# Kernel optimization log

Hardware: AMD Instinct MI355X
Metric: run time of the kernel (lower is better)

## Reference

```python
import jax, jax.numpy as jnp
import numpy as np

E = 2048
H = 16
D = E // H  # head_dim = 128


def setup_inputs() -> dict:
    key = jax.random.key(0)
    ks = jax.random.split(key, 8)
    s = 0.02
    x = jax.random.normal(ks[0], (2, 2048, E), dtype=jnp.float32)
    Wq = jax.random.normal(ks[1], (E, E), dtype=jnp.float32) * s
    Wk = jax.random.normal(ks[2], (E, E), dtype=jnp.float32) * s
    Wv = jax.random.normal(ks[3], (E, E), dtype=jnp.float32) * s
    W1 = jax.random.normal(ks[4], (2 * E, E), dtype=jnp.float32) * s
    b1 = jax.random.normal(ks[5], (2 * E,), dtype=jnp.float32) * s
    W2 = jax.random.normal(ks[6], (E, 2 * E), dtype=jnp.float32) * s
    b2 = jax.random.normal(ks[7], (E,), dtype=jnp.float32) * s
    return {"x": x, "Wq": Wq, "Wk": Wk, "Wv": Wv, "W1": W1, "b1": b1, "W2": W2, "b2": b2}


def reference(x, Wq, Wk, Wv, W1, b1, W2, b2):
    B, S, _ = x.shape
    # QKV projections (torch Linear: x @ W.T), reshape to (B,S,H,D)
    q = (x @ Wq.T).reshape(B, S, H, D)
    k = (x @ Wk.T).reshape(B, S, H, D)
    v = (x @ Wv.T).reshape(B, S, H, D)
    # scores: (B,H,S,S)
    score = jnp.einsum('bqhd,bkhd->bhqk', q, k)
    # causal mask added BEFORE scaling (as in original; -inf unaffected by scale)
    causal = jnp.tril(jnp.ones((S, S), dtype=bool))
    score = jnp.where(causal, score, -jnp.inf)
    score = score / jnp.sqrt(jnp.float32(D))
    attn = jax.nn.softmax(score, axis=-1)
    o = jnp.einsum('bhqk,bkhd->bqhd', attn, v).reshape(B, S, E)
    # FFN with hidden = 2*E, no residual connections in this block
    h = jax.nn.gelu(o @ W1.T + b1)
    return h @ W2.T + b2
```

## Files before the change

kernel.cpp:

```cpp
#include <hip/hip_runtime.h>
#include <cmath>


typedef _Float16 half8 __attribute__((ext_vector_type(8)));
typedef _Float16 half4v __attribute__((ext_vector_type(4)));
typedef float float4v __attribute__((ext_vector_type(4)));

__device__ inline void load_lds16(const _Float16* g, _Float16* l) {
  __builtin_amdgcn_global_load_lds(
      (const __attribute__((address_space(1))) void*)g,
      (__attribute__((address_space(3))) void*)l, 16, 0, 0);
}

__global__ void cvt_kernel(const float* __restrict__ s0, const float* __restrict__ s1,
                           const float* __restrict__ s2, const float* __restrict__ s3,
                           _Float16* d0, _Float16* d1, _Float16* d2, _Float16* d3,
                           int n0, int n1, int n2, int n3, float sc1) {
  const float* s;
  _Float16* d;
  int n;
  float sc = 1.0f;
  switch (blockIdx.y) {
    case 0: s = s0; d = d0; n = n0; break;
    case 1: s = s1; d = d1; n = n1; sc = sc1; break;
    case 2: s = s2; d = d2; n = n2; break;
    default: s = s3; d = d3; n = n3; break;
  }
  const int step = gridDim.x * 256 * 4;
  for (int i = (blockIdx.x * 256 + threadIdx.x) * 4; i < n; i += step) {
    float4v v = *(const float4v*)&s[i];
    half4v h;
#pragma unroll
    for (int e = 0; e < 4; e++) h[e] = (_Float16)(v[e] * sc);
    *(half4v*)&d[i] = h;
  }
}

__device__ __forceinline__ void gemm8_core(
    const _Float16* __restrict__ A, const _Float16* __restrict__ B, int K,
    int bm, int bn, _Float16* lds, float4v acc[8][4]) {
  const int tid = threadIdx.x;
  const int w = tid >> 6, lane = tid & 63;
  const int l16 = lane & 15, quad = lane >> 4;
  const int srow = w * 16 + (lane >> 2);
  const int clocal = ((lane & 3) * 8) ^ ((lane & 32) ? 16 : 0);
  int rdh = (l16 << 5) + (quad << 3);
  rdh ^= (l16 & 8) << 1;

  const _Float16* pA0 = A + (size_t)(bm + srow) * K + clocal;
  const _Float16* pA1 = A + (size_t)(bm + 128 + srow) * K + clocal;
  const _Float16* pB0 = B + (size_t)(bn + srow) * K + clocal;
  const _Float16* pB1 = B + (size_t)(bn + 128 + srow) * K + clocal;

  _Float16* const dA0 = lds + w * 1024;
  _Float16* const dA1 = lds + 8192 + w * 1024;
  _Float16* const dB0 = lds + 16384 + w * 1024;
  _Float16* const dB1 = lds + 24576 + w * 1024;

  const int aH = w >> 2, bH = (w >> 1) & 1, bRB = (w & 1) * 4;
  const _Float16* const rA0 = lds + aH * 8192;
  const _Float16* const rB0 = lds + 16384 + bH * 8192;
  const _Float16* const rA1 = rA0 + 32768;
  const _Float16* const rB1 = rB0 + 32768;

  const int NT = K >> 6;

#define STG(p, d, kt)                     \
  do {                                    \
    const _Float16* _s = (p) + (kt) * 64; \
    load_lds16(_s, (d));                  \
    load_lds16(_s + 32, (d) + 512);       \
  } while (0)
#define BARRIER() asm volatile("s_barrier" ::: "memory")
#define WAIT_LGKM()                                  \
  asm volatile("s_waitcnt lgkmcnt(0)" ::: "memory"); \
  __builtin_amdgcn_sched_barrier(0);
#define RD_A(base, RB0)                                                       \
  _Pragma("unroll") for (int rb = 0; rb < 4; rb++)                            \
  _Pragma("unroll") for (int ks = 0; ks < 2; ks++)                            \
      af[rb][ks] = *(const half8*)&(base)[((((RB0) + rb) * 2 + ks) << 9) + rdh];
#define RD_B(base, J0)                                                        \
  _Pragma("unroll") for (int j = 0; j < 2; j++)                               \
  _Pragma("unroll") for (int ks = 0; ks < 2; ks++)                            \
      bf[(J0) + j][ks] =                                                      \
          *(const half8*)&(base)[(((bRB + (J0) + j) * 2 + ks) << 9) + rdh];
#define MFMA_Q(RB0, J0)                                                       \
  __builtin_amdgcn_s_setprio(1);                                              \
  _Pragma("unroll") for (int rb = 0; rb < 4; rb++)                            \
  _Pragma("unroll") for (int j = 0; j < 2; j++)                               \
  _Pragma("unroll") for (int ks = 0; ks < 2; ks++)                            \
      acc[(RB0) + rb][(J0) + j] = __builtin_amdgcn_mfma_f32_16x16x32_f16(     \
          af[rb][ks], bf[(J0) + j][ks], acc[(RB0) + rb][(J0) + j], 0, 0, 0);  \
  __builtin_amdgcn_s_setprio(0);                                              \
  BARRIER();

  STG(pB0, dB0, 0); STG(pB1, dB1, 0); STG(pA0, dA0, 0); STG(pA1, dA1, 0);
  STG(pB0, dB0 + 32768, 1); STG(pB1, dB1 + 32768, 1);
  asm volatile("s_waitcnt vmcnt(4)" ::: "memory");
  BARRIER();

  half8 af[4][2], bf[4][2];

  for (int t = 0; t < NT; t += 2) {
    const bool last = (t + 2 >= NT);
    RD_A(rA0, 0) RD_B(rB0, 0)
    STG(pA0, dA0 + 32768, t + 1);
    BARRIER(); WAIT_LGKM()
    MFMA_Q(0, 0)
    RD_B(rB0, 2)
    STG(pA1, dA1 + 32768, t + 1);
    BARRIER(); WAIT_LGKM()
    MFMA_Q(0, 2)
    RD_A(rA0, 4)
    if (!last) STG(pB0, dB0, t + 2);
    BARRIER(); WAIT_LGKM()
    MFMA_Q(4, 0)
    if (!last) {
      STG(pA0, dA0, t + 2);
      asm volatile("s_waitcnt vmcnt(4)" ::: "memory");
    } else {
      asm volatile("s_waitcnt vmcnt(0)" ::: "memory");
    }
    BARRIER();
    MFMA_Q(4, 2)
    RD_A(rA1, 0) RD_B(rB1, 0)
    if (!last) STG(pA1, dA1, t + 2);
    BARRIER(); WAIT_LGKM()
    MFMA_Q(0, 0)
    RD_B(rB1, 2)
    if (!last) STG(pB1, dB1, t + 2);
    BARRIER(); WAIT_LGKM()
    MFMA_Q(0, 2)
    RD_A(rA1, 4)
    if (!last) STG(pB0, dB0 + 32768, t + 3);
    BARRIER(); WAIT_LGKM()
    MFMA_Q(4, 0)
    if (!last) {
      STG(pB1, dB1 + 32768, t + 3);
      asm volatile("s_waitcnt vmcnt(4)" ::: "memory");
    }
    BARRIER();
    MFMA_Q(4, 2)
  }
#undef STG
#undef BARRIER
#undef WAIT_LGKM
#undef RD_A
#undef RD_B
#undef MFMA_Q
}

__global__ __launch_bounds__(512, 2) void gemm_qkv(
    const _Float16* __restrict__ xh, const _Float16* __restrict__ Wq,
    const _Float16* __restrict__ Wk, const _Float16* __restrict__ Wv,
    _Float16* __restrict__ Qh, _Float16* __restrict__ Kh,
    _Float16* __restrict__ Vt) {
  __shared__ __align__(16) _Float16 lds[65536];
  const int z = blockIdx.z;
  const _Float16* B = (z == 0) ? Wq : (z == 1 ? Wk : Wv);
  const int bm = blockIdx.y * 256, bn = blockIdx.x * 256;
  float4v acc[8][4] = {};
  gemm8_core(xh, B, 2048, bm, bn, lds, acc);

  const int tid = threadIdx.x;
  const int w = tid >> 6, lane = tid & 63;
  const int l16 = lane & 15, quad = lane >> 4;
  const int wm = (w >> 2) * 128, wn = (w & 3) * 64;
  _Float16* outRM = z ? Kh : Qh;
#pragma unroll
  for (int j = 0; j < 4; j++) {
    const int col = bn + wn + j * 16 + l16;
#pragma unroll
    for (int rb = 0; rb < 8; rb++) {
      const int rbase = bm + wm + rb * 16 + quad * 4;
#pragma unroll
      for (int reg = 0; reg < 4; reg++) {
        const int m = rbase + reg;
        const _Float16 hv = (_Float16)acc[rb][j][reg];
        if (z == 2)
          Vt[((size_t)(m >> 11) << 22) + ((size_t)col << 11) + (m & 2047)] = hv;
        else
          outRM[(size_t)m * 2048 + col] = hv;
      }
    }
  }
}

template <bool GELU>
__global__ __launch_bounds__(512, 2) void gemm_ffn(
    const _Float16* __restrict__ A, const _Float16* __restrict__ B,
    const float* __restrict__ bias, void* __restrict__ out, int N, int K) {
  __shared__ __align__(16) _Float16 lds[65536];
  const int bm = blockIdx.y * 256, bn = blockIdx.x * 256;
  float4v acc[8][4] = {};
  gemm8_core(A, B, K, bm, bn, lds, acc);

  const int tid = threadIdx.x;
  const int w = tid >> 6, lane = tid & 63;
  const int l16 = lane & 15, quad = lane >> 4;
  const int wm = (w >> 2) * 128, wn = (w & 3) * 64;
#pragma unroll
  for (int j = 0; j < 4; j++) {
    const int col = bn + wn + j * 16 + l16;
    const float bv = bias[col];
#pragma unroll
    for (int rb = 0; rb < 8; rb++) {
      const int rbase = bm + wm + rb * 16 + quad * 4;
#pragma unroll
      for (int reg = 0; reg < 4; reg++) {
        const int m = rbase + reg;
        float v = acc[rb][j][reg] + bv;
        if (GELU) {
          const float x = v;
          const float inner = 0.7978845608028654f * (x + 0.044715f * x * x * x);
          v = 0.5f * x * (1.0f + tanhf(inner));
          ((_Float16*)out)[(size_t)m * N + col] = (_Float16)v;
        } else {
          ((float*)out)[(size_t)m * N + col] = v;
        }
      }
    }
  }
}

__global__ __launch_bounds__(256, 2) void attn_mfma(
    const _Float16* __restrict__ Qh, const _Float16* __restrict__ Kh,
    const _Float16* __restrict__ Vt, _Float16* __restrict__ Oh) {
  __shared__ __align__(16) _Float16 Ksh[64][136];
  __shared__ __align__(16) _Float16 Vsh[128][72];
  __shared__ __align__(16) _Float16 Psh[4][32][72];

  const int b = blockIdx.z;
  int qt = blockIdx.x;
  if (b) qt = gridDim.x - 1 - qt;
  const int h = blockIdx.y;
  const int tid = threadIdx.x;
  const int wave = tid >> 6, lane = tid & 63;
  const int l16 = lane & 15, quad = lane >> 4;
  const int q0 = qt * 128;
  const int wq0 = q0 + wave * 32;

  half8 qf[2][4];
#pragma unroll
  for (int rb = 0; rb < 2; rb++)
#pragma unroll
    for (int kc = 0; kc < 4; kc++)
      qf[rb][kc] = *(const half8*)(Qh +
          (size_t)(b * 2048 + wq0 + rb * 16 + l16) * 2048 + h * 128 +
          kc * 32 + quad * 8);

  half8 ones;
#pragma unroll
  for (int e = 0; e < 8; e++) ones[e] = (_Float16)1.0f;

  const int kkey = tid >> 2, kd = (tid & 3) * 32;
  const int vd = tid >> 1, vkey = (tid & 1) * 32;

  half8 kpre[4], vpre[4];
  {
    const _Float16* p = Kh + (size_t)(b * 2048 + kkey) * 2048 + h * 128 + kd;
#pragma unroll
    for (int i = 0; i < 4; i++) kpre[i] = *(const half8*)(p + i * 8);
    const _Float16* pv = Vt + ((size_t)b << 22) + (size_t)(h * 128 + vd) * 2048 + vkey;
#pragma unroll
    for (int i = 0; i < 4; i++) vpre[i] = *(const half8*)(pv + i * 8);
  }

  float4v o[2][9] = {};
  float4v mrow[2];
#pragma unroll
  for (int rb = 0; rb < 2; rb++)
#pragma unroll
    for (int e = 0; e < 4; e++) mrow[rb][e] = -INFINITY;

  const int nkb = qt * 2 + 2;
  for (int kb = 0; kb < nkb; kb++) {
    const int k0 = kb * 64;
    __syncthreads();
#pragma unroll
    for (int i = 0; i < 4; i++) *(half8*)&Ksh[kkey][kd + i * 8] = kpre[i];
#pragma unroll
    for (int i = 0; i < 4; i++) *(half8*)&Vsh[vd][vkey + i * 8] = vpre[i];
    __syncthreads();

    if (kb + 1 < nkb) {
      const int k1 = k0 + 64;
      const _Float16* p = Kh + (size_t)(b * 2048 + k1 + kkey) * 2048 + h * 128 + kd;
#pragma unroll
      for (int i = 0; i < 4; i++) kpre[i] = *(const half8*)(p + i * 8);
      const _Float16* pv = Vt + ((size_t)b << 22) + (size_t)(h * 128 + vd) * 2048 + k1 + vkey;
#pragma unroll
      for (int i = 0; i < 4; i++) vpre[i] = *(const half8*)(pv + i * 8);
    }

    if (k0 <= wq0 + 31) {
      float4v s[2][4] = {};
#pragma unroll
      for (int kc = 0; kc < 4; kc++) {
#pragma unroll
        for (int cb = 0; cb < 4; cb++) {
          half8 kf = *(const half8*)&Ksh[cb * 16 + l16][kc * 32 + quad * 8];
#pragma unroll
          for (int rb = 0; rb < 2; rb++)
            s[rb][cb] = __builtin_amdgcn_mfma_f32_16x16x32_f16(qf[rb][kc], kf, s[rb][cb], 0, 0, 0);
        }
      }
      if (k0 + 63 > wq0) {
#pragma unroll
        for (int cb = 0; cb < 4; cb++)
#pragma unroll
          for (int rb = 0; rb < 2; rb++)
#pragma unroll
            for (int reg = 0; reg < 4; reg++) {
              const int key = k0 + cb * 16 + l16;
              const int row = wq0 + rb * 16 + quad * 4 + reg;
              if (key > row) s[rb][cb][reg] = -INFINITY;
            }
      }
#pragma unroll
      for (int rb = 0; rb < 2; rb++) {
        float4v mt;
#pragma unroll
        for (int e = 0; e < 4; e++)
          mt[e] = fmaxf(fmaxf(s[rb][0][e], s[rb][1][e]),
                        fmaxf(s[rb][2][e], s[rb][3][e]));
#pragma unroll
        for (int msk = 1; msk <= 8; msk <<= 1)
#pragma unroll
          for (int e = 0; e < 4; e++) mt[e] = fmaxf(mt[e], __shfl_xor(mt[e], msk, 64));
        int need = 0;
#pragma unroll
        for (int e = 0; e < 4; e++) need |= (mt[e] > mrow[rb][e] + 8.0f) ? 1 : 0;
        if (__any(need)) {
          float4v al;
#pragma unroll
          for (int e = 0; e < 4; e++) {
            const float mn = fmaxf(mrow[rb][e], mt[e]);
            al[e] = exp2f(mrow[rb][e] - mn);
            mrow[rb][e] = mn;
          }
#pragma unroll
          for (int cd = 0; cd < 9; cd++)
#pragma unroll
            for (int e = 0; e < 4; e++) o[rb][cd][e] *= al[e];
        }
#pragma unroll
        for (int cb = 0; cb < 4; cb++) {
#pragma unroll
          for (int e = 0; e < 4; e++) s[rb][cb][e] = exp2f(s[rb][cb][e] - mrow[rb][e]);
#pragma unroll
          for (int e = 0; e < 4; e++)
            Psh[wave][rb * 16 + quad * 4 + e][cb * 16 + l16] = (_Float16)s[rb][cb][e];
        }
      }
      half8 pf[2][2];
#pragma unroll
      for (int rb = 0; rb < 2; rb++)
#pragma unroll
        for (int kc = 0; kc < 2; kc++)
          pf[rb][kc] = *(const half8*)&Psh[wave][rb * 16 + l16][kc * 32 + quad * 8];
#pragma unroll
      for (int cd = 0; cd < 8; cd++) {
#pragma unroll
        for (int kc = 0; kc < 2; kc++) {
          half8 vf = *(const half8*)&Vsh[cd * 16 + l16][kc * 32 + quad * 8];
#pragma unroll
          for (int rb = 0; rb < 2; rb++)
            o[rb][cd] = __builtin_amdgcn_mfma_f32_16x16x32_f16(pf[rb][kc], vf, o[rb][cd], 0, 0, 0);
        }
      }
#pragma unroll
      for (int kc = 0; kc < 2; kc++)
#pragma unroll
        for (int rb = 0; rb < 2; rb++)
          o[rb][8] = __builtin_amdgcn_mfma_f32_16x16x32_f16(pf[rb][kc], ones, o[rb][8], 0, 0, 0);
    }
  }

#pragma unroll
  for (int rb = 0; rb < 2; rb++) {
    float4v inv;
#pragma unroll
    for (int e = 0; e < 4; e++) inv[e] = 1.0f / o[rb][8][e];
#pragma unroll
    for (int cd = 0; cd < 8; cd++)
#pragma unroll
      for (int reg = 0; reg < 4; reg++)
        Oh[(size_t)(b * 2048 + wq0 + rb * 16 + quad * 4 + reg) * 2048 +
           h * 128 + cd * 16 + l16] = (_Float16)(o[rb][cd][reg] * inv[reg]);
  }
}

extern "C" void kernel_launch(void* const* d_in, const int* in_sizes, int n_in,
                              void* d_out, int out_size, void* d_ws,
                              size_t ws_size, hipStream_t stream) {
  const float* x = (const float*)d_in[0];
  const float* Wq = (const float*)d_in[1];
  const float* Wk = (const float*)d_in[2];
  const float* Wv = (const float*)d_in[3];
  const float* W1 = (const float*)d_in[4];
  const float* b1 = (const float*)d_in[5];
  const float* W2 = (const float*)d_in[6];
  const float* b2 = (const float*)d_in[7];
  float* out = (float*)d_out;

  const int ME = 8388608;
  const int EE = 4194304;

  _Float16* ws = (_Float16*)d_ws;
  _Float16* xh  = ws;
  _Float16* Wqh = xh + ME;
  _Float16* Wkh = Wqh + EE;
  _Float16* Wvh = Wkh + EE;
  _Float16* Qh  = Wvh + EE;
  _Float16* Kh  = Qh + ME;
  _Float16* Vt  = Kh + ME;
  _Float16* Oh  = xh;
  _Float16* W1h = Wqh;
  _Float16* W2h = Vt;
  _Float16* Hid = Qh;

  const float qscale = 1.4426950408889634f * 0.08838834764831845f;

  cvt_kernel<<<dim3(1024, 4), 256, 0, stream>>>(x, Wq, Wk, Wv, xh, Wqh, Wkh, Wvh,
                                                ME, EE, EE, EE, qscale);
  gemm_qkv<<<dim3(8, 16, 3), 512, 0, stream>>>(xh, Wqh, Wkh, Wvh, Qh, Kh, Vt);
  attn_mfma<<<dim3(16, 16, 2), 256, 0, stream>>>(Qh, Kh, Vt, Oh);
  cvt_kernel<<<dim3(1024, 2), 256, 0, stream>>>(W1, W2, nullptr, nullptr,
                                                W1h, W2h, nullptr, nullptr,
                                                ME, ME, 0, 0, 1.0f);
  gemm_ffn<true><<<dim3(16, 16), 512, 0, stream>>>(Oh, W1h, b1, Hid, 4096, 2048);
  gemm_ffn<false><<<dim3(8, 16), 512, 0, stream>>>(Hid, W2h, b2, out, 2048, 4096);
}
```

Baseline: 601.6 us.

## Restructure GEMM pipeline with double-buffered fragments, XCD tile swizzle, LDS-staged V transpose

Rewrites the GEMM main loop to keep low and high register fragment sets, so LDS reads for the next MFMA quarter overlap the current one. It uses partial lgkmcnt waits and fewer barriers, and issues global-to-LDS copies in pairs. Block indices are remapped so consecutive tiles land on the same XCD for L2 reuse. The V projection epilogue now transposes through padded LDS and writes vectorised rows instead of scattered scalar stores, at the cost of extra registers and a slightly larger LDS allocation.

Result: slower. 671.0 us (+11.5%).

```diff
diff --git a/kernel.cpp b/kernel.cpp
--- a/kernel.cpp
+++ b/kernel.cpp
@@ -36,6 +36,36 @@
   }
 }
 
+#define STG2(p, d, kt)                    \
+  do {                                    \
+    const _Float16* _s = (p) + (kt) * 64; \
+    load_lds16(_s, (d));                  \
+    load_lds16(_s + 32, (d) + 512);       \
+  } while (0)
+#define BAR() asm volatile("s_barrier" ::: "memory")
+#define SB0() __builtin_amdgcn_sched_barrier(0)
+#define VM0() asm volatile("s_waitcnt vmcnt(0)" ::: "memory")
+#define WAITL(N)                                          \
+  asm volatile("s_waitcnt lgkmcnt(" #N ")" ::: "memory"); \
+  __builtin_amdgcn_sched_barrier(0);
+#define RD_AF(dst, base, RB0)                                                \
+  _Pragma("unroll") for (int rb = 0; rb < 4; rb++)                           \
+  _Pragma("unroll") for (int ks = 0; ks < 2; ks++)                           \
+      dst[rb][ks] = *(const half8*)&(base)[((((RB0) + rb) * 2 + ks) << 9) + rdh];
+#define RD_BF(dst, base, J0)                                                 \
+  _Pragma("unroll") for (int j = 0; j < 2; j++)                              \
+  _Pragma("unroll") for (int ks = 0; ks < 2; ks++)                           \
+      dst[j][ks] =                                                           \
+          *(const half8*)&(base)[(((bRB + (J0) + j) * 2 + ks) << 9) + rdh];
+#define MFMA16(AF, BF, RB0, J0)                                              \
+  __builtin_amdgcn_s_setprio(1);                                             \
+  _Pragma("unroll") for (int rb = 0; rb < 4; rb++)                           \
+  _Pragma("unroll") for (int j = 0; j < 2; j++)                              \
+  _Pragma("unroll") for (int ks = 0; ks < 2; ks++)                           \
+      acc[(RB0) + rb][(J0) + j] = __builtin_amdgcn_mfma_f32_16x16x32_f16(    \
+          AF[rb][ks], BF[j][ks], acc[(RB0) + rb][(J0) + j], 0, 0, 0);        \
+  __builtin_amdgcn_s_setprio(0);
+
 __device__ __forceinline__ void gemm8_core(
     const _Float16* __restrict__ A, const _Float16* __restrict__ B, int K,
     int bm, int bn, _Float16* lds, float4v acc[8][4]) {
@@ -58,96 +88,79 @@
   _Float16* const dB1 = lds + 24576 + w * 1024;
 
   const int aH = w >> 2, bH = (w >> 1) & 1, bRB = (w & 1) * 4;
-  const _Float16* const rA0 = lds + aH * 8192;
-  const _Float16* const rB0 = lds + 16384 + bH * 8192;
-  const _Float16* const rA1 = rA0 + 32768;
-  const _Float16* const rB1 = rB0 + 32768;
+  const _Float16* const rA = lds + aH * 8192;
+  const _Float16* const rB = lds + 16384 + bH * 8192;
+  const _Float16* const rAn = rA + 32768;
+  const _Float16* const rBn = rB + 32768;
 
   const int NT = K >> 6;
 
-#define STG(p, d, kt)                     \
-  do {                                    \
-    const _Float16* _s = (p) + (kt) * 64; \
-    load_lds16(_s, (d));                  \
-    load_lds16(_s + 32, (d) + 512);       \
-  } while (0)
-#define BARRIER() asm volatile("s_barrier" ::: "memory")
-#define WAIT_LGKM()                                  \
-  asm volatile("s_waitcnt lgkmcnt(0)" ::: "memory"); \
-  __builtin_amdgcn_sched_barrier(0);
-#define RD_A(base, RB0)                                                       \
-  _Pragma("unroll") for (int rb = 0; rb < 4; rb++)                            \
-  _Pragma("unroll") for (int ks = 0; ks < 2; ks++)                            \
-      af[rb][ks] = *(const half8*)&(base)[((((RB0) + rb) * 2 + ks) << 9) + rdh];
-#define RD_B(base, J0)                                                        \
-  _Pragma("unroll") for (int j = 0; j < 2; j++)                               \
-  _Pragma("unroll") for (int ks = 0; ks < 2; ks++)                            \
-      bf[(J0) + j][ks] =                                                      \
-          *(const half8*)&(base)[(((bRB + (J0) + j) * 2 + ks) << 9) + rdh];
-#define MFMA_Q(RB0, J0)                                                       \
-  __builtin_amdgcn_s_setprio(1);                                              \
-  _Pragma("unroll") for (int rb = 0; rb < 4; rb++)                            \
-  _Pragma("unroll") for (int j = 0; j < 2; j++)                               \
-  _Pragma("unroll") for (int ks = 0; ks < 2; ks++)                            \
-      acc[(RB0) + rb][(J0) + j] = __builtin_amdgcn_mfma_f32_16x16x32_f16(     \
-          af[rb][ks], bf[(J0) + j][ks], acc[(RB0) + rb][(J0) + j], 0, 0, 0);  \
-  __builtin_amdgcn_s_setprio(0);                                              \
-  BARRIER();
-
-  STG(pB0, dB0, 0); STG(pB1, dB1, 0); STG(pA0, dA0, 0); STG(pA1, dA1, 0);
-  STG(pB0, dB0 + 32768, 1); STG(pB1, dB1 + 32768, 1);
+  half8 afLo[4][2], afHi[4][2], bfLo[2][2], bfHi[2][2];
+
+  STG2(pB0, dB0, 0); STG2(pB1, dB1, 0); STG2(pA0, dA0, 0); STG2(pA1, dA1, 0);
+  STG2(pB0, dB0 + 32768, 1); STG2(pB1, dB1 + 32768, 1);
   asm volatile("s_waitcnt vmcnt(4)" ::: "memory");
-  BARRIER();
-
-  half8 af[4][2], bf[4][2];
+  BAR();
+  RD_AF(afLo, rA, 0) RD_BF(bfLo, rB, 0)
+  STG2(pA0, dA0 + 32768, 1); STG2(pA1, dA1 + 32768, 1);
 
   for (int t = 0; t < NT; t += 2) {
-    const bool last = (t + 2 >= NT);
-    RD_A(rA0, 0) RD_B(rB0, 0)
-    STG(pA0, dA0 + 32768, t + 1);
-    BARRIER(); WAIT_LGKM()
-    MFMA_Q(0, 0)
-    RD_B(rB0, 2)
-    STG(pA1, dA1 + 32768, t + 1);
-    BARRIER(); WAIT_LGKM()
-    MFMA_Q(0, 2)
-    RD_A(rA0, 4)
-    if (!last) STG(pB0, dB0, t + 2);
-    BARRIER(); WAIT_LGKM()
-    MFMA_Q(4, 0)
-    if (!last) {
-      STG(pA0, dA0, t + 2);
-      asm volatile("s_waitcnt vmcnt(4)" ::: "memory");
+    const bool lastg = (t + 2 >= NT);
+    RD_BF(bfHi, rB, 2)
+    WAITL(4)
+    MFMA16(afLo, bfLo, 0, 0)
+    BAR();
+    RD_AF(afHi, rA, 4)
+    WAITL(8)
+    MFMA16(afLo, bfHi, 0, 2)
+    VM0();
+    BAR();
+    RD_AF(afLo, rAn, 0)
+    if (!lastg) { STG2(pB0, dB0, t + 2); STG2(pB1, dB1, t + 2); }
+    WAITL(8)
+    MFMA16(afHi, bfLo, 4, 0)
+    BAR();
+    RD_BF(bfLo, rBn, 0)
+    if (!lastg) { STG2(pA0, dA0, t + 2); STG2(pA1, dA1, t + 2); }
+    SB0();
+    MFMA16(afHi, bfHi, 4, 2)
+    BAR();
+    RD_BF(bfHi, rBn, 2)
+    WAITL(4)
+    MFMA16(afLo, bfLo, 0, 0)
+    BAR();
+    RD_AF(afHi, rAn, 4)
+    WAITL(8)
+    MFMA16(afLo, bfHi, 0, 2)
+    VM0();
+    BAR();
+    if (!lastg) {
+      RD_AF(afLo, rA, 0)
+      STG2(pB0, dB0 + 32768, t + 3); STG2(pB1, dB1 + 32768, t + 3);
+      WAITL(8)
     } else {
-      asm volatile("s_waitcnt vmcnt(0)" ::: "memory");
-    }
-    BARRIER();
-    MFMA_Q(4, 2)
-    RD_A(rA1, 0) RD_B(rB1, 0)
-    if (!last) STG(pA1, dA1, t + 2);
-    BARRIER(); WAIT_LGKM()
-    MFMA_Q(0, 0)
-    RD_B(rB1, 2)
-    if (!last) STG(pB1, dB1, t + 2);
-    BARRIER(); WAIT_LGKM()
-    MFMA_Q(0, 2)
-    RD_A(rA1, 4)
-    if (!last) STG(pB0, dB0 + 32768, t + 3);
-    BARRIER(); WAIT_LGKM()
-    MFMA_Q(4, 0)
-    if (!last) {
-      STG(pB1, dB1 + 32768, t + 3);
-      asm volatile("s_waitcnt vmcnt(4)" ::: "memory");
-    }
-    BARRIER();
-    MFMA_Q(4, 2)
-  }
-#undef STG
-#undef BARRIER
-#undef WAIT_LGKM
-#undef RD_A
-#undef RD_B
-#undef MFMA_Q
+      WAITL(0)
+    }
+    MFMA16(afHi, bfLo, 4, 0)
+    BAR();
+    if (!lastg) {
+      RD_BF(bfLo, rB, 0)
+      STG2(pA0, dA0 + 32768, t + 3); STG2(pA1, dA1 + 32768, t + 3);
+    }
+    SB0();
+    MFMA16(afHi, bfHi, 4, 2)
+    BAR();
+  }
+}
+
+__device__ __forceinline__ void xcd_tile(int& bm, int& bn) {
+  const int nx = gridDim.x;
+  const int nwg = nx * gridDim.y;
+  const int lin = blockIdx.x + nx * blockIdx.y;
+  const int cpx = nwg >> 3;
+  const int s = (lin & 7) * cpx + (lin >> 3);
+  bm = (s / nx) * 256;
+  bn = (s % nx) * 256;
 }
 
 __global__ __launch_bounds__(512, 2) void gemm_qkv(
@@ -155,10 +168,11 @@
     const _Float16* __restrict__ Wk, const _Float16* __restrict__ Wv,
     _Float16* __restrict__ Qh, _Float16* __restrict__ Kh,
     _Float16* __restrict__ Vt) {
-  __shared__ __align__(16) _Float16 lds[65536];
+  __shared__ __align__(16) _Float16 lds[67584];
   const int z = blockIdx.z;
   const _Float16* B = (z == 0) ? Wq : (z == 1 ? Wk : Wv);
-  const int bm = blockIdx.y * 256, bn = blockIdx.x * 256;
+  int bm, bn;
+  xcd_tile(bm, bn);
   float4v acc[8][4] = {};
   gemm8_core(xh, B, 2048, bm, bn, lds, acc);
 
@@ -166,21 +180,40 @@
   const int w = tid >> 6, lane = tid & 63;
   const int l16 = lane & 15, quad = lane >> 4;
   const int wm = (w >> 2) * 128, wn = (w & 3) * 64;
-  _Float16* outRM = z ? Kh : Qh;
-#pragma unroll
-  for (int j = 0; j < 4; j++) {
-    const int col = bn + wn + j * 16 + l16;
-#pragma unroll
-    for (int rb = 0; rb < 8; rb++) {
-      const int rbase = bm + wm + rb * 16 + quad * 4;
-#pragma unroll
-      for (int reg = 0; reg < 4; reg++) {
-        const int m = rbase + reg;
-        const _Float16 hv = (_Float16)acc[rb][j][reg];
-        if (z == 2)
-          Vt[((size_t)(m >> 11) << 22) + ((size_t)col << 11) + (m & 2047)] = hv;
-        else
-          outRM[(size_t)m * 2048 + col] = hv;
+  if (z == 2) {
+    _Float16* Tr = lds;
+    __syncthreads();
+#pragma unroll
+    for (int j = 0; j < 4; j++) {
+      const int cl = wn + j * 16 + l16;
+#pragma unroll
+      for (int rb = 0; rb < 8; rb++) {
+        const int ml = wm + rb * 16 + quad * 4;
+#pragma unroll
+        for (int reg = 0; reg < 4; reg++)
+          Tr[cl * 264 + ml + reg] = (_Float16)acc[rb][j][reg];
+      }
+    }
+    __syncthreads();
+    const int cl = tid >> 1;
+    const int ml = (tid & 1) * 128;
+    const int mg = bm + ml;
+    _Float16* dst = Vt + ((size_t)(mg >> 11) << 22) +
+                    ((size_t)(bn + cl) << 11) + (mg & 2047);
+#pragma unroll
+    for (int i = 0; i < 16; i++)
+      *(half8*)(dst + i * 8) = *(const half8*)&Tr[cl * 264 + ml + i * 8];
+  } else {
+    _Float16* outRM = z ? Kh : Qh;
+#pragma unroll
+    for (int j = 0; j < 4; j++) {
+      const int col = bn + wn + j * 16 + l16;
+#pragma unroll
+      for (int rb = 0; rb < 8; rb++) {
+        const int rbase = bm + wm + rb * 16 + quad * 4;
+#pragma unroll
+        for (int reg = 0; reg < 4; reg++)
+          outRM[(size_t)(rbase + reg) * 2048 + col] = (_Float16)acc[rb][j][reg];
       }
     }
   }
@@ -191,7 +224,8 @@
     const _Float16* __restrict__ A, const _Float16* __restrict__ B,
     const float* __restrict__ bias, void* __restrict__ out, int N, int K) {
   __shared__ __align__(16) _Float16 lds[65536];
-  const int bm = blockIdx.y * 256, bn = blockIdx.x * 256;
+  int bm, bn;
+  xcd_tile(bm, bn);
   float4v acc[8][4] = {};
   gemm8_core(A, B, K, bm, bn, lds, acc);
 
```

## Split-K the second FFN GEMM and stage V-transpose stores through LDS

Applied to the files above, without the earlier changes.

The second FFN GEMM (K=4096) is split into two K-halves launched as a z=2 grid. This doubles the block count from 128 to 256 so the GPU is better filled, and a reduce kernel then sums the partials with the bias. Separately, the V projection epilogue now transposes its tile through LDS so it can write Vt with coalesced 16-byte stores instead of scattered 2-byte ones. The costs are an extra kernel launch, 32 MB of extra fp32 partial traffic, and a larger LDS allocation in gemm_qkv that could affect occupancy.

After: 546.9 us. 1.1x faster.

```diff
diff --git a/kernel.cpp b/kernel.cpp
--- a/kernel.cpp
+++ b/kernel.cpp
@@ -37,8 +37,8 @@
 }
 
 __device__ __forceinline__ void gemm8_core(
-    const _Float16* __restrict__ A, const _Float16* __restrict__ B, int K,
-    int bm, int bn, _Float16* lds, float4v acc[8][4]) {
+    const _Float16* __restrict__ A, const _Float16* __restrict__ B, int Kloop,
+    int Kstride, int bm, int bn, _Float16* lds, float4v acc[8][4]) {
   const int tid = threadIdx.x;
   const int w = tid >> 6, lane = tid & 63;
   const int l16 = lane & 15, quad = lane >> 4;
@@ -47,10 +47,10 @@
   int rdh = (l16 << 5) + (quad << 3);
   rdh ^= (l16 & 8) << 1;
 
-  const _Float16* pA0 = A + (size_t)(bm + srow) * K + clocal;
-  const _Float16* pA1 = A + (size_t)(bm + 128 + srow) * K + clocal;
-  const _Float16* pB0 = B + (size_t)(bn + srow) * K + clocal;
-  const _Float16* pB1 = B + (size_t)(bn + 128 + srow) * K + clocal;
+  const _Float16* pA0 = A + (size_t)(bm + srow) * Kstride + clocal;
+  const _Float16* pA1 = A + (size_t)(bm + 128 + srow) * Kstride + clocal;
+  const _Float16* pB0 = B + (size_t)(bn + srow) * Kstride + clocal;
+  const _Float16* pB1 = B + (size_t)(bn + 128 + srow) * Kstride + clocal;
 
   _Float16* const dA0 = lds + w * 1024;
   _Float16* const dA1 = lds + 8192 + w * 1024;
@@ -63,7 +63,7 @@
   const _Float16* const rA1 = rA0 + 32768;
   const _Float16* const rB1 = rB0 + 32768;
 
-  const int NT = K >> 6;
+  const int NT = Kloop >> 6;
 
 #define STG(p, d, kt)                     \
   do {                                    \
@@ -155,45 +155,63 @@
     const _Float16* __restrict__ Wk, const _Float16* __restrict__ Wv,
     _Float16* __restrict__ Qh, _Float16* __restrict__ Kh,
     _Float16* __restrict__ Vt) {
-  __shared__ __align__(16) _Float16 lds[65536];
+  __shared__ __align__(16) _Float16 lds[67584];
   const int z = blockIdx.z;
   const _Float16* B = (z == 0) ? Wq : (z == 1 ? Wk : Wv);
   const int bm = blockIdx.y * 256, bn = blockIdx.x * 256;
   float4v acc[8][4] = {};
-  gemm8_core(xh, B, 2048, bm, bn, lds, acc);
+  gemm8_core(xh, B, 2048, 2048, bm, bn, lds, acc);
 
   const int tid = threadIdx.x;
   const int w = tid >> 6, lane = tid & 63;
   const int l16 = lane & 15, quad = lane >> 4;
   const int wm = (w >> 2) * 128, wn = (w & 3) * 64;
-  _Float16* outRM = z ? Kh : Qh;
-#pragma unroll
-  for (int j = 0; j < 4; j++) {
-    const int col = bn + wn + j * 16 + l16;
-#pragma unroll
-    for (int rb = 0; rb < 8; rb++) {
-      const int rbase = bm + wm + rb * 16 + quad * 4;
-#pragma unroll
-      for (int reg = 0; reg < 4; reg++) {
-        const int m = rbase + reg;
-        const _Float16 hv = (_Float16)acc[rb][j][reg];
-        if (z == 2)
-          Vt[((size_t)(m >> 11) << 22) + ((size_t)col << 11) + (m & 2047)] = hv;
-        else
-          outRM[(size_t)m * 2048 + col] = hv;
-      }
-    }
-  }
-}
-
-template <bool GELU>
-__global__ __launch_bounds__(512, 2) void gemm_ffn(
+  if (z == 2) {
+    _Float16* Tr = lds;
+    __syncthreads();
+#pragma unroll
+    for (int j = 0; j < 4; j++) {
+      const int cl = wn + j * 16 + l16;
+#pragma unroll
+      for (int rb = 0; rb < 8; rb++) {
+        const int ml = wm + rb * 16 + quad * 4;
+#pragma unroll
+        for (int reg = 0; reg < 4; reg++)
+          Tr[cl * 264 + ml + reg] = (_Float16)acc[rb][j][reg];
+      }
+    }
+    __syncthreads();
+    const int cl = tid >> 1;
+    const int ml = (tid & 1) * 128;
+    const int mg = bm + ml;
+    _Float16* dst = Vt + ((size_t)(mg >> 11) << 22) +
+                    ((size_t)(bn + cl) << 11) + (mg & 2047);
+#pragma unroll
+    for (int i = 0; i < 16; i++)
+      *(half8*)(dst + i * 8) = *(const half8*)&Tr[cl * 264 + ml + i * 8];
+  } else {
+    _Float16* outRM = z ? Kh : Qh;
+#pragma unroll
+    for (int j = 0; j < 4; j++) {
+      const int col = bn + wn + j * 16 + l16;
+#pragma unroll
+      for (int rb = 0; rb < 8; rb++) {
+        const int rbase = bm + wm + rb * 16 + quad * 4;
+#pragma unroll
+        for (int reg = 0; reg < 4; reg++)
+          outRM[(size_t)(rbase + reg) * 2048 + col] = (_Float16)acc[rb][j][reg];
+      }
+    }
+  }
+}
+
+__global__ __launch_bounds__(512, 2) void gemm_ffn1(
     const _Float16* __restrict__ A, const _Float16* __restrict__ B,
-    const float* __restrict__ bias, void* __restrict__ out, int N, int K) {
+    const float* __restrict__ bias, _Float16* __restrict__ out, int N, int K) {
   __shared__ __align__(16) _Float16 lds[65536];
   const int bm = blockIdx.y * 256, bn = blockIdx.x * 256;
   float4v acc[8][4] = {};
-  gemm8_core(A, B, K, bm, bn, lds, acc);
+  gemm8_core(A, B, K, K, bm, bn, lds, acc);
 
   const int tid = threadIdx.x;
   const int w = tid >> 6, lane = tid & 63;
@@ -209,17 +227,52 @@
 #pragma unroll
       for (int reg = 0; reg < 4; reg++) {
         const int m = rbase + reg;
-        float v = acc[rb][j][reg] + bv;
-        if (GELU) {
-          const float x = v;
-          const float inner = 0.7978845608028654f * (x + 0.044715f * x * x * x);
-          v = 0.5f * x * (1.0f + tanhf(inner));
-          ((_Float16*)out)[(size_t)m * N + col] = (_Float16)v;
-        } else {
-          ((float*)out)[(size_t)m * N + col] = v;
-        }
-      }
-    }
+        const float x = acc[rb][j][reg] + bv;
+        const float inner = 0.7978845608028654f * (x + 0.044715f * x * x * x);
+        out[(size_t)m * N + col] = (_Float16)(0.5f * x * (1.0f + tanhf(inner)));
+      }
+    }
+  }
+}
+
+__global__ __launch_bounds__(512, 2) void gemm_ffn2_part(
+    const _Float16* __restrict__ A, const _Float16* __restrict__ B,
+    float* __restrict__ p0, float* __restrict__ p1) {
+  __shared__ __align__(16) _Float16 lds[65536];
+  const int bm = blockIdx.y * 256, bn = blockIdx.x * 256;
+  const int k0 = blockIdx.z * 2048;
+  float* out = blockIdx.z ? p1 : p0;
+  float4v acc[8][4] = {};
+  gemm8_core(A + k0, B + k0, 2048, 4096, bm, bn, lds, acc);
+
+  const int tid = threadIdx.x;
+  const int w = tid >> 6, lane = tid & 63;
+  const int l16 = lane & 15, quad = lane >> 4;
+  const int wm = (w >> 2) * 128, wn = (w & 3) * 64;
+#pragma unroll
+  for (int j = 0; j < 4; j++) {
+    const int col = bn + wn + j * 16 + l16;
+#pragma unroll
+    for (int rb = 0; rb < 8; rb++) {
+      const int rbase = bm + wm + rb * 16 + quad * 4;
+#pragma unroll
+      for (int reg = 0; reg < 4; reg++)
+        out[(size_t)(rbase + reg) * 2048 + col] = acc[rb][j][reg];
+    }
+  }
+}
+
+__global__ void reduce_add(float* __restrict__ out, const float* __restrict__ p0,
+                           const float* __restrict__ b2, int n) {
+  const int step = gridDim.x * 256 * 4;
+  for (int i = (blockIdx.x * 256 + threadIdx.x) * 4; i < n; i += step) {
+    float4v a = *(const float4v*)&out[i];
+    float4v b = *(const float4v*)&p0[i];
+    float4v bb = *(const float4v*)&b2[i & 2047];
+    float4v r;
+#pragma unroll
+    for (int e = 0; e < 4; e++) r[e] = a[e] + b[e] + bb[e];
+    *(float4v*)&out[i] = r;
   }
 }
 
@@ -419,6 +472,7 @@
   _Float16* W1h = Wqh;
   _Float16* W2h = Vt;
   _Float16* Hid = Qh;
+  float*    P0  = (float*)ws;
 
   const float qscale = 1.4426950408889634f * 0.08838834764831845f;
 
@@ -429,6 +483,7 @@
   cvt_kernel<<<dim3(1024, 2), 256, 0, stream>>>(W1, W2, nullptr, nullptr,
                                                 W1h, W2h, nullptr, nullptr,
                                                 ME, ME, 0, 0, 1.0f);
-  gemm_ffn<true><<<dim3(16, 16), 512, 0, stream>>>(Oh, W1h, b1, Hid, 4096, 2048);
-  gemm_ffn<false><<<dim3(8, 16), 512, 0, stream>>>(Hid, W2h, b2, out, 2048, 4096);
-}
+  gemm_ffn1<<<dim3(16, 16), 512, 0, stream>>>(Oh, W1h, b1, Hid, 4096, 2048);
+  gemm_ffn2_part<<<dim3(8, 16, 2), 512, 0, stream>>>(Hid, W2h, P0, out);
+  reduce_add<<<dim3(2048), 256, 0, stream>>>(out, P0, b2, ME);
+}
```
